# Optimization experiments

Measured on AMD Instinct MI355X. Metric: run time of the kernel, lower is better.

Reference implementation:

```python
import math
import jax, jax.numpy as jnp
import numpy as np

EPS = 1e-6
PI = math.pi


def _normalize(x):
    n = jnp.linalg.norm(x, axis=-1, keepdims=True)
    return x / jnp.maximum(n, 1e-12)


def _envmap_samples(W, H):
    # linspace(0.5/H, 1-0.5/H, H) == (arange(H)+0.5)/H
    v = (jnp.arange(H, dtype=jnp.float32) + 0.5) / H
    u = (jnp.arange(W, dtype=jnp.float32) + 0.5) / W
    uu, vv = jnp.meshgrid(u, v, indexing='xy')          # (H, W)
    uv = jnp.stack([uu, vv], axis=-1)                    # (H, W, 2)
    phi = uv[..., 0] * 2 * PI + PI / 2
    theta = uv[..., 1] * PI
    dirs = jnp.stack([jnp.sin(theta) * jnp.cos(phi),
                      jnp.cos(theta),
                      -jnp.sin(theta) * jnp.sin(phi)], axis=-1)
    sa = jnp.sin(theta) * (PI / H) * (2 * PI / W)
    M = W * H
    return dirs.reshape(M, 3), sa.reshape(M, 1), uv.reshape(M, 2)


def _grid_sample_bilinear(img, uv):
    # img: (B, C, H, W); uv: (M, 2) in [0,1]; torch grid_sample align_corners=False, border pad
    B, C, H, W = img.shape
    g = uv * 2.0 - 1.0
    x = ((g[:, 0] + 1.0) * W - 1.0) / 2.0
    y = ((g[:, 1] + 1.0) * H - 1.0) / 2.0
    x0 = jnp.floor(x); y0 = jnp.floor(y)
    wx = (x - x0)[None, None, :]
    wy = (y - y0)[None, None, :]
    x0i = jnp.clip(x0, 0, W - 1).astype(jnp.int32)
    x1i = jnp.clip(x0 + 1, 0, W - 1).astype(jnp.int32)
    y0i = jnp.clip(y0, 0, H - 1).astype(jnp.int32)
    y1i = jnp.clip(y0 + 1, 0, H - 1).astype(jnp.int32)
    flat = img.reshape(B, C, H * W)
    def gather(yi, xi):
        return jnp.take(flat, yi * W + xi, axis=2)       # (B, C, M)
    v00 = gather(y0i, x0i); v01 = gather(y0i, x1i)
    v10 = gather(y1i, x0i); v11 = gather(y1i, x1i)
    return (v00 * (1 - wx) + v01 * wx) * (1 - wy) + (v10 * (1 - wx) + v11 * wx) * wy


def _forward(points_normals, points_albedo, points_metallic, points_smoothness,
             viewing_dirs, env_vis, env_map):
    B, N, V, _ = viewing_dirs.shape
    _, W, H, _ = env_map.shape
    n = _normalize(points_normals)            # (B, N, 3)
    v = _normalize(viewing_dirs)              # (B, N, V, 3)
    roughness = 1.0 - points_smoothness       # (B, N, 1)

    l_dirs, sa, uvs = _envmap_samples(W, H)   # (M,3), (M,1), (M,2)
    img = jnp.transpose(env_map, (0, 3, 2, 1))              # (B, 3, H, W)
    Li = jnp.transpose(_grid_sample_bilinear(img, uvs), (0, 2, 1))  # (B, M, 3)

    # broadcast everything to (B, N, V, M, ...)
    n_e = n[:, :, None, None, :]
    v_e = v[:, :, :, None, :]
    l_e = l_dirs[None, None, None, :, :]
    Li_e = Li[:, None, None, :, :]
    vis_e = env_vis[:, :, None, :, None]
    sa_e = sa[None, None, None, :, :]
    alb = points_albedo[:, :, None, None, :]
    met = points_metallic[:, :, None, None, :]
    rough = roughness[:, :, None, None, :]
    f0 = 0.04 + (alb - 0.04) * met            # lerp(0.04, albedo, metallic)

    h = _normalize(v_e + l_e)
    NdotL = jnp.maximum(jnp.sum(n_e * l_e, -1, keepdims=True), EPS)
    NdotV = jnp.maximum(jnp.sum(n_e * v_e, -1, keepdims=True), EPS)
    NdotH = jnp.maximum(jnp.sum(n_e * h, -1, keepdims=True), 0.0)
    VdotH = jnp.maximum(jnp.sum(l_e * h, -1, keepdims=True), 0.0)

    Fr = f0 + (1.0 - f0) * jnp.power(1.0 - jnp.clip(VdotH, 0.0, 1.0), 5.0)
    alpha = rough * rough
    alpha2 = alpha * alpha
    denom = NdotH * NdotH * (alpha2 - 1.0) + 1.0
    D = alpha2 / (PI * denom * denom + EPS)
    k = alpha / 2.0
    G = (NdotV / (NdotV * (1.0 - k) + k + EPS)) * (NdotL / (NdotL * (1.0 - k) + k + EPS))
    spec = Fr * D * G / (4.0 * NdotV * NdotL + EPS)
    diffuse = (1.0 - Fr) * (1.0 - met) * (alb / PI)
    brdf = diffuse + spec
    radiance = brdf * (Li_e * vis_e) * NdotL * sa_e       # (B, N, V, M, 3)
    return jnp.sum(radiance, axis=3)                      # (B, N, V, 3)


def setup_inputs() -> dict:
    key = jax.random.key(0)
    ks = jax.random.split(key, 7)
    B, N, V, W, H = 1, 4096, 2, 32, 16
    M = W * H
    return {
        'points_normals': jax.random.normal(ks[0], (B, N, 3), dtype=jnp.float32),
        'points_albedo': jax.random.uniform(ks[1], (B, N, 3), dtype=jnp.float32),
        'points_metallic': jax.random.uniform(ks[2], (B, N, 1), dtype=jnp.float32),
        'points_smoothness': jax.random.uniform(ks[3], (B, N, 1), dtype=jnp.float32),
        'viewing_dirs': jax.random.normal(ks[4], (B, N, V, 3), dtype=jnp.float32),
        'env_vis': jax.random.uniform(ks[5], (B, N, M), dtype=jnp.float32),
        'env_map': jax.random.uniform(ks[6], (B, W, H, 3), dtype=jnp.float32),
    }


def reference(points_normals, points_albedo, points_metallic, points_smoothness,
              viewing_dirs, env_vis, env_map):
    return _forward(points_normals, points_albedo, points_metallic,
                    points_smoothness, viewing_dirs, env_vis, env_map)
```

## Files before the change

kernel.cpp:

```cpp
#include <hip/hip_runtime.h>
#include <math.h>

#define PI_F 3.14159265358979323846f
#define EPS_F 1e-6f


__global__ __launch_bounds__(256) void hdr_render_kernel(
    const float* __restrict__ normals,
    const float* __restrict__ albedo,
    const float* __restrict__ metallic,
    const float* __restrict__ smooth,
    const float* __restrict__ vdirs,
    const float* __restrict__ env_vis,
    const float* __restrict__ env_map,
    float* __restrict__ out,
    int N)
{
    __shared__ float s_lx[512], s_ly[512], s_lz[512];
    __shared__ float s_L0[512], s_L1[512], s_L2[512];

    const int tid = threadIdx.x;

    for (int m = tid; m < 512; m += 256) {
        const int x = m & 31;
        const int y = m >> 5;
        const float u  = (x + 0.5f) * (1.0f / 32.0f);
        const float vv = (y + 0.5f) * (1.0f / 16.0f);
        const float phi   = u * (2.0f * PI_F) + 0.5f * PI_F;
        const float theta = vv * PI_F;
        float st, ct, sp, cp;
        sincosf(theta, &st, &ct);
        sincosf(phi,   &sp, &cp);
        const float sa = st * (PI_F / 16.0f) * (2.0f * PI_F / 32.0f);
        const int base = (x * 16 + y) * 3;
        const int sw = (m & 7) * 64 + (m >> 3);
        s_lx[sw] = st * cp;
        s_ly[sw] = ct;
        s_lz[sw] = -st * sp;
        s_L0[sw] = env_map[base + 0] * sa;
        s_L1[sw] = env_map[base + 1] * sa;
        s_L2[sw] = env_map[base + 2] * sa;
    }
    __syncthreads();

    const int lane = tid & 63;
    const int wave = tid >> 6;
    const int n = blockIdx.x * 4 + wave;
    if (n >= N) return;

    float nx = normals[n * 3 + 0];
    float ny = normals[n * 3 + 1];
    float nz = normals[n * 3 + 2];
    {
        const float inv = 1.0f / fmaxf(sqrtf(nx*nx + ny*ny + nz*nz), 1e-12f);
        nx *= inv; ny *= inv; nz *= inv;
    }
    float vx0 = vdirs[n * 6 + 0], vy0 = vdirs[n * 6 + 1], vz0 = vdirs[n * 6 + 2];
    float vx1 = vdirs[n * 6 + 3], vy1 = vdirs[n * 6 + 4], vz1 = vdirs[n * 6 + 5];
    {
        const float inv = 1.0f / fmaxf(sqrtf(vx0*vx0 + vy0*vy0 + vz0*vz0), 1e-12f);
        vx0 *= inv; vy0 *= inv; vz0 *= inv;
    }
    {
        const float inv = 1.0f / fmaxf(sqrtf(vx1*vx1 + vy1*vy1 + vz1*vz1), 1e-12f);
        vx1 *= inv; vy1 *= inv; vz1 *= inv;
    }
    const float alb0 = albedo[n * 3 + 0];
    const float alb1 = albedo[n * 3 + 1];
    const float alb2 = albedo[n * 3 + 2];
    const float met  = metallic[n];
    const float sm   = smooth[n];

    const float rough  = 1.0f - sm;
    const float alpha  = rough * rough;
    const float alpha2 = alpha * alpha;
    const float a2m1   = alpha2 - 1.0f;
    const float k      = 0.5f * alpha;
    const float omk    = 1.0f - k;
    const float kpe    = k + EPS_F;

    const float NdotV0 = fmaxf(nx*vx0 + ny*vy0 + nz*vz0, EPS_F);
    const float NdotV1 = fmaxf(nx*vx1 + ny*vy1 + nz*vz1, EPS_F);
    const float gv0 = NdotV0 / (NdotV0 * omk + kpe);
    const float gv1 = NdotV1 / (NdotV1 * omk + kpe);
    const float c1v0 = alpha2 * gv0;
    const float c1v1 = alpha2 * gv1;
    const float fNV0 = 4.0f * NdotV0;
    const float fNV1 = 4.0f * NdotV1;

    const float f00 = 0.04f + (alb0 - 0.04f) * met;
    const float f01 = 0.04f + (alb1 - 0.04f) * met;
    const float f02 = 0.04f + (alb2 - 0.04f) * met;
    const float omf00 = 1.0f - f00, omf01 = 1.0f - f01, omf02 = 1.0f - f02;
    const float db0 = (1.0f - met) * alb0 * (1.0f / PI_F);
    const float db1 = (1.0f - met) * alb1 * (1.0f / PI_F);
    const float db2 = (1.0f - met) * alb2 * (1.0f / PI_F);

    const float* __restrict__ visrow = env_vis + (size_t)n * 512 + lane * 8;
    const float4 vA = *(const float4*)(visrow);
    const float4 vB = *(const float4*)(visrow + 4);
    const float vis[8] = { vA.x, vA.y, vA.z, vA.w, vB.x, vB.y, vB.z, vB.w };

    float a00 = 0.f, a01 = 0.f, a02 = 0.f;
    float a10 = 0.f, a11 = 0.f, a12 = 0.f;

    #pragma unroll
    for (int i = 0; i < 8; ++i) {
        const int idx = i * 64 + lane;
        const float lx = s_lx[idx];
        const float ly = s_ly[idx];
        const float lz = s_lz[idx];

        const float NdotL = fmaxf(fmaf(nx, lx, fmaf(ny, ly, nz * lz)), EPS_F);
        const float glden = fmaf(NdotL, omk, kpe);
        const float w  = vis[i] * NdotL;
        const float t0 = s_L0[idx] * w;
        const float t1 = s_L1[idx] * w;
        const float t2 = s_L2[idx] * w;

        {
            const float hx = vx0 + lx, hy = vy0 + ly, hz = vz0 + lz;
            const float h2 = fmaf(hx, hx, fmaf(hy, hy, hz * hz));
            const float hinv = __builtin_amdgcn_rsqf(fmaxf(h2, 1e-24f));
            const float nh = fmaf(nx, hx, fmaf(ny, hy, nz * hz));
            const float lh = fmaf(lx, hx, fmaf(ly, hy, lz * hz));
            const float NdotH = fmaxf(nh * hinv, 0.0f);
            const float VdotH = fmaxf(lh * hinv, 0.0f);
            const float p  = 1.0f - fminf(VdotH, 1.0f);
            const float p2 = p * p;
            const float p5 = p2 * p2 * p;
            const float dn   = fmaf(NdotH * NdotH, a2m1, 1.0f);
            const float Dden = fmaf(PI_F * dn, dn, EPS_F);
            const float sden = fmaf(fNV0, NdotL, EPS_F);
            const float sfac = c1v0 * NdotL * __builtin_amdgcn_rcpf(Dden * glden * sden);
            const float Fr0 = fmaf(omf00, p5, f00);
            const float Fr1 = fmaf(omf01, p5, f01);
            const float Fr2 = fmaf(omf02, p5, f02);
            a00 = fmaf(fmaf(Fr0, sfac, db0 * (1.0f - Fr0)), t0, a00);
            a01 = fmaf(fmaf(Fr1, sfac, db1 * (1.0f - Fr1)), t1, a01);
            a02 = fmaf(fmaf(Fr2, sfac, db2 * (1.0f - Fr2)), t2, a02);
        }
        {
            const float hx = vx1 + lx, hy = vy1 + ly, hz = vz1 + lz;
            const float h2 = fmaf(hx, hx, fmaf(hy, hy, hz * hz));
            const float hinv = __builtin_amdgcn_rsqf(fmaxf(h2, 1e-24f));
            const float nh = fmaf(nx, hx, fmaf(ny, hy, nz * hz));
            const float lh = fmaf(lx, hx, fmaf(ly, hy, lz * hz));
            const float NdotH = fmaxf(nh * hinv, 0.0f);
            const float VdotH = fmaxf(lh * hinv, 0.0f);
            const float p  = 1.0f - fminf(VdotH, 1.0f);
            const float p2 = p * p;
            const float p5 = p2 * p2 * p;
            const float dn   = fmaf(NdotH * NdotH, a2m1, 1.0f);
            const float Dden = fmaf(PI_F * dn, dn, EPS_F);
            const float sden = fmaf(fNV1, NdotL, EPS_F);
            const float sfac = c1v1 * NdotL * __builtin_amdgcn_rcpf(Dden * glden * sden);
            const float Fr0 = fmaf(omf00, p5, f00);
            const float Fr1 = fmaf(omf01, p5, f01);
            const float Fr2 = fmaf(omf02, p5, f02);
            a10 = fmaf(fmaf(Fr0, sfac, db0 * (1.0f - Fr0)), t0, a10);
            a11 = fmaf(fmaf(Fr1, sfac, db1 * (1.0f - Fr1)), t1, a11);
            a12 = fmaf(fmaf(Fr2, sfac, db2 * (1.0f - Fr2)), t2, a12);
        }
    }

    #pragma unroll
    for (int off = 32; off >= 1; off >>= 1) {
        a00 += __shfl_down(a00, off, 64);
        a01 += __shfl_down(a01, off, 64);
        a02 += __shfl_down(a02, off, 64);
        a10 += __shfl_down(a10, off, 64);
        a11 += __shfl_down(a11, off, 64);
        a12 += __shfl_down(a12, off, 64);
    }

    if (lane == 0) {
        float* o = out + (size_t)n * 6;
        o[0] = a00; o[1] = a01; o[2] = a02;
        o[3] = a10; o[4] = a11; o[5] = a12;
    }
}

extern "C" void kernel_launch(void* const* d_in, const int* in_sizes, int n_in,
                              void* d_out, int out_size, void* d_ws, size_t ws_size,
                              hipStream_t stream) {
    const float* normals  = (const float*)d_in[0];
    const float* albedo   = (const float*)d_in[1];
    const float* metallic = (const float*)d_in[2];
    const float* smooth   = (const float*)d_in[3];
    const float* vdirs    = (const float*)d_in[4];
    const float* env_vis  = (const float*)d_in[5];
    const float* env_map  = (const float*)d_in[6];
    float* out = (float*)d_out;

    const int N = in_sizes[0] / 3;
    const int blocks = (N + 3) / 4;

    hdr_render_kernel<<<blocks, 256, 0, stream>>>(
        normals, albedo, metallic, smooth, vdirs, env_vis, env_map, out, N);
}
```

Baseline: 76.28 us.

## Use sine table for envmap dirs, 512-thread blocks, fold Fresnel blend, vector stores

Replaces the per-block sincosf setup with a small constant sine table indexed by symmetry, and doubles the block size to 512 threads (8 points per block) so each thread sets up exactly one envmap sample and the setup cost is spread over more points. The specular/diffuse blend is rewritten as Fr*(sfac-db)+db, saving a multiply per channel. Output stores become float2 writes. The table values are hardcoded for the 32x16 envmap, and larger blocks may change occupancy and scheduling.

```diff
diff --git a/kernel.cpp b/kernel.cpp
--- a/kernel.cpp
+++ b/kernel.cpp
@@ -5,7 +5,7 @@
 #define EPS_F 1e-6f
 
 
-__global__ __launch_bounds__(256) void hdr_render_kernel(
+__global__ __launch_bounds__(512) void hdr_render_kernel(
     const float* __restrict__ normals,
     const float* __restrict__ albedo,
     const float* __restrict__ metallic,
@@ -21,22 +21,31 @@
 
     const int tid = threadIdx.x;
 
-    for (int m = tid; m < 512; m += 256) {
+    {
+        static const float S8[8] = {
+            0.09801714f, 0.29028468f, 0.47139674f, 0.63439328f,
+            0.77301045f, 0.88192126f, 0.95694034f, 0.99518473f };
+
+        const int m = tid;
         const int x = m & 31;
         const int y = m >> 5;
-        const float u  = (x + 0.5f) * (1.0f / 32.0f);
-        const float vv = (y + 0.5f) * (1.0f / 16.0f);
-        const float phi   = u * (2.0f * PI_F) + 0.5f * PI_F;
-        const float theta = vv * PI_F;
-        float st, ct, sp, cp;
-        sincosf(theta, &st, &ct);
-        sincosf(phi,   &sp, &cp);
-        const float sa = st * (PI_F / 16.0f) * (2.0f * PI_F / 32.0f);
+
+        const float st = S8[(y < 8) ? y : (15 - y)];
+        float ct = S8[(y < 8) ? (7 - y) : (y - 8)];
+        if (y >= 8) ct = -ct;
+
+        const int q = x >> 3, r = x & 7;
+        float sin_a = S8[(q & 1) ? (7 - r) : r];
+        if (q >= 2) sin_a = -sin_a;
+        float cos_a = S8[(q & 1) ? r : (7 - r)];
+        if (q == 1 || q == 2) cos_a = -cos_a;
+
+        const float sa = st * ((PI_F / 16.0f) * (2.0f * PI_F / 32.0f));
         const int base = (x * 16 + y) * 3;
         const int sw = (m & 7) * 64 + (m >> 3);
-        s_lx[sw] = st * cp;
+        s_lx[sw] = -st * sin_a;
         s_ly[sw] = ct;
-        s_lz[sw] = -st * sp;
+        s_lz[sw] = -st * cos_a;
         s_L0[sw] = env_map[base + 0] * sa;
         s_L1[sw] = env_map[base + 1] * sa;
         s_L2[sw] = env_map[base + 2] * sa;
@@ -45,7 +54,7 @@
 
     const int lane = tid & 63;
     const int wave = tid >> 6;
-    const int n = blockIdx.x * 4 + wave;
+    const int n = blockIdx.x * 8 + wave;
     if (n >= N) return;
 
     float nx = normals[n * 3 + 0];
@@ -133,12 +142,15 @@
             const float Dden = fmaf(PI_F * dn, dn, EPS_F);
             const float sden = fmaf(fNV0, NdotL, EPS_F);
             const float sfac = c1v0 * NdotL * __builtin_amdgcn_rcpf(Dden * glden * sden);
+            const float sd0 = sfac - db0;
+            const float sd1 = sfac - db1;
+            const float sd2 = sfac - db2;
             const float Fr0 = fmaf(omf00, p5, f00);
             const float Fr1 = fmaf(omf01, p5, f01);
             const float Fr2 = fmaf(omf02, p5, f02);
-            a00 = fmaf(fmaf(Fr0, sfac, db0 * (1.0f - Fr0)), t0, a00);
-            a01 = fmaf(fmaf(Fr1, sfac, db1 * (1.0f - Fr1)), t1, a01);
-            a02 = fmaf(fmaf(Fr2, sfac, db2 * (1.0f - Fr2)), t2, a02);
+            a00 = fmaf(fmaf(Fr0, sd0, db0), t0, a00);
+            a01 = fmaf(fmaf(Fr1, sd1, db1), t1, a01);
+            a02 = fmaf(fmaf(Fr2, sd2, db2), t2, a02);
         }
         {
             const float hx = vx1 + lx, hy = vy1 + ly, hz = vz1 + lz;
@@ -155,12 +167,15 @@
             const float Dden = fmaf(PI_F * dn, dn, EPS_F);
             const float sden = fmaf(fNV1, NdotL, EPS_F);
             const float sfac = c1v1 * NdotL * __builtin_amdgcn_rcpf(Dden * glden * sden);
+            const float sd0 = sfac - db0;
+            const float sd1 = sfac - db1;
+            const float sd2 = sfac - db2;
             const float Fr0 = fmaf(omf00, p5, f00);
             const float Fr1 = fmaf(omf01, p5, f01);
             const float Fr2 = fmaf(omf02, p5, f02);
-            a10 = fmaf(fmaf(Fr0, sfac, db0 * (1.0f - Fr0)), t0, a10);
-            a11 = fmaf(fmaf(Fr1, sfac, db1 * (1.0f - Fr1)), t1, a11);
-            a12 = fmaf(fmaf(Fr2, sfac, db2 * (1.0f - Fr2)), t2, a12);
+            a10 = fmaf(fmaf(Fr0, sd0, db0), t0, a10);
+            a11 = fmaf(fmaf(Fr1, sd1, db1), t1, a11);
+            a12 = fmaf(fmaf(Fr2, sd2, db2), t2, a12);
         }
     }
 
@@ -176,8 +191,9 @@
 
     if (lane == 0) {
         float* o = out + (size_t)n * 6;
-        o[0] = a00; o[1] = a01; o[2] = a02;
-        o[3] = a10; o[4] = a11; o[5] = a12;
+        *(float2*)(o + 0) = make_float2(a00, a01);
+        *(float2*)(o + 2) = make_float2(a02, a10);
+        *(float2*)(o + 4) = make_float2(a11, a12);
     }
 }
 
@@ -194,8 +210,8 @@
     float* out = (float*)d_out;
 
     const int N = in_sizes[0] / 3;
-    const int blocks = (N + 3) / 4;
-
-    hdr_render_kernel<<<blocks, 256, 0, stream>>>(
+    const int blocks = (N + 7) / 8;
+
+    hdr_render_kernel<<<blocks, 512, 0, stream>>>(
         normals, albedo, metallic, smooth, vdirs, env_vis, env_map, out, N);
 }
```

Result: slower. 77.98 us (+2.2%).
